# Kernel tuning notes

Hardware: AMD Instinct MI355X
Metric: run time of the kernel (lower is better)

Reference implementation:

```python
import jax, jax.numpy as jnp
import numpy as np

N_NODES = 15
K = 5
L_IN = 1920
C_OUT = 256
L3 = L_IN - 3 * K + 3  # 1908
EPS = 1e-5


def setup_inputs() -> dict:
    key = jax.random.key(0)
    ks = jax.random.split(key, 18)
    B, E = 128, 56
    s = 0.05
    inp = {
        'X': jax.random.normal(ks[0], (B, N_NODES, L_IN), jnp.float32),
        'edge_index': jax.random.randint(ks[1], (2, E), 0, N_NODES),
        'edge_weight': jax.random.uniform(ks[2], (E,), jnp.float32),
        # grouped conv params (groups = N_NODES): per-group channels 1->16->32->1
        'conv1_w': jax.random.normal(ks[3], (16 * N_NODES, 1, K), jnp.float32) * s,
        'conv1_b': jnp.zeros((16 * N_NODES,), jnp.float32),
        'conv2_w': jax.random.normal(ks[4], (32 * N_NODES, 16, K), jnp.float32) * s,
        'conv2_b': jnp.zeros((32 * N_NODES,), jnp.float32),
        'conv3_w': jax.random.normal(ks[5], (N_NODES, 32, K), jnp.float32) * s,
        'conv3_b': jnp.zeros((N_NODES,), jnp.float32),
        # GCNConv: lin weight [out,in] + bias
        'gcn_w': jax.random.normal(ks[6], (C_OUT, L3), jnp.float32) * s,
        'gcn_b': jnp.zeros((C_OUT,), jnp.float32),
        'lin1_w': jax.random.normal(ks[7], (C_OUT, L_IN), jnp.float32) * s,
        'lin1_b': jnp.zeros((C_OUT,), jnp.float32),
        # GraphNorm params
        'gn_w': jnp.ones((C_OUT,), jnp.float32),
        'gn_b': jnp.zeros((C_OUT,), jnp.float32),
        'gn_ms': jnp.ones((C_OUT,), jnp.float32),
        'out_w': jax.random.normal(ks[8], (16, C_OUT), jnp.float32) * s,
        'out_b': jnp.zeros((16,), jnp.float32),
    }
    return inp


def _gconv(x, w, b):
    # grouped valid conv1d, NCH layout
    y = jax.lax.conv_general_dilated(
        x, w, window_strides=(1,), padding='VALID',
        dimension_numbers=('NCH', 'OIH', 'NCH'),
        feature_group_count=N_NODES)
    return y + b[None, :, None]


def _gcn(x, edge_index, edge_weight, W, b):
    # x: [B, N, L3]; batched GCNConv with shared edge structure (no per-t loop)
    src, dst = edge_index[0], edge_index[1]
    loop = jnp.arange(N_NODES)
    src = jnp.concatenate([src, loop])
    dst = jnp.concatenate([dst, loop])
    ew = jnp.concatenate([edge_weight, jnp.ones((N_NODES,), edge_weight.dtype)])
    deg = jnp.zeros((N_NODES,), ew.dtype).at[dst].add(ew)  # in-degree on target
    dinv = jnp.where(deg > 0, jax.lax.rsqrt(deg), 0.0)
    norm = dinv[src] * ew * dinv[dst]  # [E']
    xl = jnp.einsum('bnf,of->bno', x, W)  # [B, N, C_OUT]
    msg = norm[None, :, None] * xl[:, src, :]  # [B, E', C_OUT]
    out = jnp.zeros_like(xl).at[:, dst, :].add(msg)
    return out + b


def reference(X, edge_index, edge_weight, conv1_w, conv1_b, conv2_w, conv2_b,
              conv3_w, conv3_b, gcn_w, gcn_b, lin1_w, lin1_b, gn_w, gn_b,
              gn_ms, out_w, out_b):
    h = jax.nn.leaky_relu(_gconv(X, conv1_w, conv1_b), 0.01)
    h = jax.nn.leaky_relu(_gconv(h, conv2_w, conv2_b), 0.01)
    h = jax.nn.leaky_relu(_gconv(h, conv3_w, conv3_b), 0.01)  # [B, N, L3]
    T = _gcn(h, edge_index, edge_weight, gcn_w, gcn_b)  # [B, N, C_OUT]
    # GraphNorm with batch=None -> single graph over dim 0
    mean = T.mean(axis=0, keepdims=True)
    out = T - mean * gn_ms
    var = (out * out).mean(axis=0, keepdims=True)
    T = gn_w * out / jnp.sqrt(var + EPS) + gn_b
    T = jax.nn.elu(T + jnp.einsum('bnl,ol->bno', X, lin1_w) + lin1_b)
    output = T.mean(axis=1)  # global_mean_pool over nodes -> [B, C_OUT]
    class_output = output @ out_w.T + out_b  # [B, 16]
    return (output, class_output)
```

## Files before the change

kernel.cpp:

```cpp
#include <hip/hip_runtime.h>

typedef unsigned short u16;
typedef unsigned int   u32;

typedef short shortx8   __attribute__((ext_vector_type(8)));
typedef float floatx4   __attribute__((ext_vector_type(4)));
typedef float floatx16  __attribute__((ext_vector_type(16)));
typedef u32   uintx2    __attribute__((ext_vector_type(2)));
typedef u32   uintx4    __attribute__((ext_vector_type(4)));

typedef u32     u32a     __attribute__((may_alias));
typedef uintx2  uintx2a  __attribute__((may_alias));
typedef uintx4  uintx4a  __attribute__((may_alias));
typedef shortx8 shortx8a __attribute__((may_alias));

__device__ __forceinline__ u16 f2bf(float f){
  union { float f; u32 i; } v; v.f = f;
  return (u16)((v.i + 0x7fffu + ((v.i >> 16) & 1u)) >> 16);
}
__device__ __forceinline__ u16 f2bf_fast(float f){
  union { float f; u32 i; } v; v.f = f;
  return (u16)((v.i + 0x8000u) >> 16);
}
__device__ __forceinline__ u32 pack2(float lo, float hi){
  union { float f; u32 i; } a, b; a.f = lo; b.f = hi;
  return __builtin_amdgcn_perm(b.i + 0x8000u, a.i + 0x8000u, 0x07060302u);
}
__device__ __forceinline__ u32 cvtpk2(float lo, float hi){
#if __has_builtin(__builtin_amdgcn_cvt_pk_bf16_f32)
  auto pv = __builtin_amdgcn_cvt_pk_bf16_f32(lo, hi);
  if constexpr (sizeof(pv) == 4){
    u32 out; __builtin_memcpy(&out, &pv, 4); return out;
  } else {
    return pack2(lo, hi);
  }
#else
  return pack2(lo, hi);
#endif
}
__device__ __forceinline__ float lrelu(float v){ return fmaxf(v, 0.01f*v); }

__global__ void __launch_bounds__(256, 4) fused_conv(
    const float* __restrict__ X,
    const float* __restrict__ w1, const float* __restrict__ b1,
    const float* __restrict__ w2, const float* __restrict__ b2,
    const float* __restrict__ w3, const float* __restrict__ b3,
    u16* __restrict__ h3p, u16* __restrict__ Xb,
    const float* __restrict__ lw, u16* __restrict__ lwb,
    const float* __restrict__ gw, u16* __restrict__ gwp,
    float* __restrict__ xlz, float* __restrict__ l1z){
  const int tid  = threadIdx.x;
  const int node = blockIdx.z;
  const int p0   = blockIdx.x * 120;
  const int b0   = blockIdx.y * 8;

  __shared__ __attribute__((aligned(16))) u16 sPair[2][4352];
  __shared__ __attribute__((aligned(16))) u16 sW2f[2560];
  __shared__ __attribute__((aligned(16))) u16 sW3f[160];
  __shared__ __attribute__((aligned(16))) u16 sXb[8*136];
  __shared__ float sW1[80], sB1[16], sB2[32];

  {
    const int bid = blockIdx.x + 16*(blockIdx.y + 16*blockIdx.z);
    int gid = bid*256 + tid;
    if (gid < 491520){
      lwb[gid] = f2bf(lw[gid]);
      xlz[gid] = 0.f;
    } else {
      int g2 = gid - 491520;
      int row = g2 / 1920;
      int col = g2 - row*1920;
      gwp[g2] = (col < 1908) ? f2bf(gw[row*1908 + col]) : (u16)0;
      l1z[g2] = 0.f;
    }
  }

  {
    const int bls = tid >> 5, i0 = tid & 31;
    const float* xrow = X  + (size_t)((b0 + bls)*15 + node)*1920;
    u16*        xbrow = Xb + (size_t)((b0 + bls)*15 + node)*1920;
    #pragma unroll
    for (int u = 0; u < 5; ++u){
      int i = i0 + 32*u;
      if (i < 136){
        int g = p0 + i;
        float xv = (g < 1920) ? xrow[g] : 0.f;
        u16 xb = f2bf_fast(xv);
        sXb[bls*136 + i] = xb;
        if (i < 120) xbrow[g] = xb;
      }
    }
    #pragma unroll
    for (int u = 0; u < 10; ++u){
      int d = tid + 256*u;
      int j = d & 7, oc = (d >> 3) & 31, kh = (d >> 8) & 1, tap = d >> 9;
      sW2f[d] = f2bf(w2[node*2560 + (oc*16 + kh*8 + j)*5 + tap]);
    }
    if (tid < 160){
      int icc = tid / 5, tp = tid - 5*icc;
      sW3f[tp*32 + icc] = f2bf(w3[node*160 + tid]);
    }
    if (tid < 80) sW1[tid] = w1[node*80 + tid];
    if (tid < 16) sB1[tid] = b1[node*16 + tid];
    if (tid < 32) sB2[tid] = b2[node*32 + tid];
    {
      const int pr = tid >> 7, idx = tid & 127;
      sPair[pr][1632 + (64 + (idx >> 5))*40 + (idx & 31)] = 0;
    }
  }
  __syncthreads();

  const int w = tid >> 6, lane = tid & 63;
  const int pw = w >> 1, ph = w & 1;
  const int m = lane & 15, quad = lane >> 4;
  const int t32 = lane & 31, kh = lane >> 5;

  shortx8 a2t[5];
  #pragma unroll
  for (int tap = 0; tap < 5; ++tap)
    a2t[tap] = *(const shortx8a*)&sW2f[((tap*2 + kh)*32 + t32)*8];

  float biasr[16];
  #pragma unroll
  for (int r = 0; r < 16; ++r)
    biasr[r] = sB2[(r&3) + 8*(r>>2) + 4*kh];

  shortx8 a3[5];
  {
    const shortx8 zv = {0,0,0,0,0,0,0,0};
    #pragma unroll
    for (int tp = 0; tp < 5; ++tp){
      shortx8 t = *(const shortx8a*)&sW3f[tp*32 + quad*8];
      a3[tp] = (m == 0) ? t : zv;
    }
  }
  const float b3v = b3[node];

  shortx8 a1h = {0,0,0,0,0,0,0,0}, a1l = {0,0,0,0,0,0,0,0};
  if (quad == 0){
    const float* wrow = sW1 + m*5;
    #pragma unroll
    for (int j = 0; j < 5; ++j){
      float wv = wrow[j];
      u16 h = f2bf(wv);
      union { u32 i; float f; } hf; hf.i = ((u32)h) << 16;
      u16 l = f2bf(wv - hf.f);
      a1h[j] = (short)h; a1l[j] = (short)l;
    }
  }
  float biasA[4];
  #pragma unroll
  for (int r = 0; r < 4; ++r) biasA[r] = sB1[quad*4 + r];

  u16* h1w = sPair[pw];
  u16* h2w = sPair[pw] + 1632;

  for (int bb = 0; bb < 4; ++bb){
    const int bl = pw + bb*2;
    const int rg = (b0 + bl)*15 + node;

    {
      const int s = tid & 127;
      if (s < 68){
        const u32* xb32 = (const u32*)sXb + bl*68;
        u32 r0 = xb32[s];
        u32 r1 = (s+1 < 68) ? xb32[s+1] : 0u;
        u32 r2 = (s+2 < 68) ? xb32[s+2] : 0u;
        u32 r3 = (s+3 < 68) ? xb32[s+3] : 0u;
        u32 r4 = (s+4 < 68) ? xb32[s+4] : 0u;
        const int te = 2*s, to = 2*s + 1;
        const int offE = (s < 34) ? te*24 + 16 : 1632 + (te - 68)*40 + 32;
        const int offO = (s < 34) ? to*24 + 16 : 1632 + (to - 68)*40 + 32;
        uintx4 ve = {r0, r1, r2, r3};
        uintx4 vo = {__builtin_amdgcn_alignbit(r1, r0, 16),
                     __builtin_amdgcn_alignbit(r2, r1, 16),
                     __builtin_amdgcn_alignbit(r3, r2, 16),
                     __builtin_amdgcn_alignbit(r4, r3, 16)};
        *(uintx4a*)(h1w + offE) = ve;
        *(uintx4a*)(h1w + offO) = vo;
      }
    }
    __syncthreads();

    #pragma unroll
    for (int tt = 0; tt < 2; ++tt){
      const int p = p0 + tt*60;

      #pragma unroll
      for (int ti = 0; ti < 3; ++ti){
        const int T = ph + 2*ti;
        if (T < 5){
          const int tr = T*16 + m;
          int row = tt*60 + tr;
          row = row > 135 ? 135 : row;
          shortx8 bfr = {0,0,0,0,0,0,0,0};
          if (quad == 0){
            const int off = (row < 68) ? row*24 + 16 : 1632 + (row - 68)*40 + 32;
            bfr = *(const shortx8a*)(h1w + off);
          }
          floatx4 acc = {biasA[0], biasA[1], biasA[2], biasA[3]};
          acc = __builtin_amdgcn_mfma_f32_16x16x32_bf16(a1l, bfr, acc, 0, 0, 0);
          acc = __builtin_amdgcn_mfma_f32_16x16x32_bf16(a1h, bfr, acc, 0, 0, 0);
          if (tr < 68){
            uintx2 pk = { cvtpk2(lrelu(acc[0]), lrelu(acc[1])),
                          cvtpk2(lrelu(acc[2]), lrelu(acc[3])) };
            *(uintx2a*)(h1w + tr*24 + quad*4) = pk;
          }
        }
      }
      __syncthreads();

      {
        const int t0 = ph*32;
        floatx16 acc;
        #pragma unroll
        for (int r = 0; r < 16; ++r) acc[r] = biasr[r];
        #pragma unroll
        for (int tap = 0; tap < 5; ++tap){
          shortx8 bfr = *(const shortx8a*)(h1w + (t0 + t32 + tap)*24 + kh*8);
          acc = __builtin_amdgcn_mfma_f32_32x32x16_bf16(a2t[tap], bfr, acc, 0, 0, 0);
        }
        u16* dst = h2w + (t0 + t32)*40;
        #pragma unroll
        for (int r = 0; r < 16; r += 2){
          float v0 = lrelu(acc[r]);
          float v1 = lrelu(acc[r+1]);
          const int oc0 = (r&3) + 8*(r>>2) + 4*kh;
          *(u32a*)(dst + oc0) = cvtpk2(v0, v1);
        }
      }
      __syncthreads();

      #pragma unroll
      for (int i = 0; i < 2; ++i){
        const int nt = 2*ph + i;
        floatx4 acc3 = {0.f,0.f,0.f,0.f};
        if (lane < 16) acc3[0] = b3v;
        #pragma unroll
        for (int tp = 0; tp < 5; ++tp){
          shortx8 bfr = *(const shortx8a*)(h2w + (nt*16 + m + tp)*40 + quad*8);
          acc3 = __builtin_amdgcn_mfma_f32_16x16x32_bf16(a3[tp], bfr, acc3, 0, 0, 0);
        }
        const int tl = nt*16 + lane;
        if (lane < 16 && tl < 60){
          const int t3 = p + tl;
          float v = lrelu(acc3[0]);
          h3p[(size_t)rg*1920 + t3] = (t3 < 1908) ? f2bf_fast(v) : (u16)0;
        }
      }
    }
  }
}

__global__ void __launch_bounds__(256) gemm_nt(
    const u16* __restrict__ A0, const u16* __restrict__ B0, float* __restrict__ O0,
    const u16* __restrict__ A1, const u16* __restrict__ B1, float* __restrict__ O1,
    float* __restrict__ gZ){
  const int job = blockIdx.z >> 1, khf = blockIdx.z & 1;
  const u16* A; const u16* Bm; float* O;
  if (job == 0){ A = A0; Bm = B0; O = O0; } else { A = A1; Bm = B1; O = O1; }
  __shared__ __attribute__((aligned(16))) u16 sA[2][64*88];
  __shared__ __attribute__((aligned(16))) u16 sB[2][64*88];
  const int tid = threadIdx.x;
  if (blockIdx.x == 0 && blockIdx.y == 0 && blockIdx.z == 0){
    #pragma unroll
    for (int u = 0; u < 30; ++u) gZ[tid + 256*u] = 0.f;
  }
  const int m0 = blockIdx.x*64, n0 = blockIdx.y*64;
  const int row = tid >> 2, kc = tid & 3;
  const int w = tid >> 6, lane = tid & 63;
  const int m = lane & 15, quad = lane >> 4;
  const int mo = (w & 1)*32, no = (w >> 1)*32;
  floatx4 acc[2][2];
  #pragma unroll
  for (int i = 0; i < 2; ++i)
    #pragma unroll
    for (int j = 0; j < 2; ++j)
      #pragma unroll
      for (int r = 0; r < 4; ++r) acc[i][j][r] = 0.f;

  const u16* ap = A  + (size_t)(m0 + row)*1920 + khf*960 + kc*8;
  const u16* bp = Bm + (size_t)(n0 + row)*1920 + khf*960 + kc*8;
  uintx4 va0 = *(const uintx4a*)ap;
  uintx4 va1 = *(const uintx4a*)(ap + 32);
  uintx4 vb0 = *(const uintx4a*)bp;
  uintx4 vb1 = *(const uintx4a*)(bp + 32);
  ap += 64; bp += 64;

  for (int kt = 0; kt < 15; ++kt){
    const int c = kt & 1;
    *(uintx4a*)&sA[c][row*88 + kc*8]      = va0;
    *(uintx4a*)&sA[c][row*88 + 32 + kc*8] = va1;
    *(uintx4a*)&sB[c][row*88 + kc*8]      = vb0;
    *(uintx4a*)&sB[c][row*88 + 32 + kc*8] = vb1;
    __syncthreads();
    if (kt < 14){
      va0 = *(const uintx4a*)ap;
      va1 = *(const uintx4a*)(ap + 32);
      vb0 = *(const uintx4a*)bp;
      vb1 = *(const uintx4a*)(bp + 32);
      ap += 64; bp += 64;
    }
    #pragma unroll
    for (int ks = 0; ks < 64; ks += 32){
      const shortx8 af0 = *(const shortx8a*)&sA[c][(mo      + m)*88 + ks + quad*8];
      const shortx8 af1 = *(const shortx8a*)&sA[c][(mo + 16 + m)*88 + ks + quad*8];
      const shortx8 bf0 = *(const shortx8a*)&sB[c][(no      + m)*88 + ks + quad*8];
      const shortx8 bf1 = *(const shortx8a*)&sB[c][(no + 16 + m)*88 + ks + quad*8];
      acc[0][0] = __builtin_amdgcn_mfma_f32_16x16x32_bf16(af0, bf0, acc[0][0], 0, 0, 0);
      acc[0][1] = __builtin_amdgcn_mfma_f32_16x16x32_bf16(af0, bf1, acc[0][1], 0, 0, 0);
      acc[1][0] = __builtin_amdgcn_mfma_f32_16x16x32_bf16(af1, bf0, acc[1][0], 0, 0, 0);
      acc[1][1] = __builtin_amdgcn_mfma_f32_16x16x32_bf16(af1, bf1, acc[1][1], 0, 0, 0);
    }
  }
  #pragma unroll
  for (int mi = 0; mi < 2; ++mi)
    #pragma unroll
    for (int ni = 0; ni < 2; ++ni)
      #pragma unroll
      for (int r = 0; r < 4; ++r){
        int rr = m0 + mo + mi*16 + quad*4 + r;
        int cc = n0 + no + ni*16 + m;
        atomicAdd(&O[(size_t)rr*256 + cc], acc[mi][ni][r]);
      }
}

__global__ void __launch_bounds__(256) gcn_agg(
    const float* __restrict__ xl, const int* __restrict__ ei,
    const float* __restrict__ ew, const float* __restrict__ gcn_b,
    float* __restrict__ Tpre, float* __restrict__ gS, float* __restrict__ gS2){
  const int b = blockIdx.x, tid = threadIdx.x;
  __shared__ float sxl[15*256];
  __shared__ float s_deg[15], s_dinv[15], s_norm[71];
  __shared__ int   s_cnt[15], s_start[16], s_fill[15], s_srcl[71];
  if (tid < 15){ s_deg[tid] = 0.f; s_cnt[tid] = 0; s_fill[tid] = 0; }
  #pragma unroll
  for (int n = 0; n < 15; ++n)
    sxl[n*256 + tid] = xl[(size_t)(b*15 + n)*256 + tid];
  __syncthreads();
  int se = 0, de = 0; float we = 0.f;
  if (tid < 71){
    if (tid < 56){ se = ei[tid]; de = ei[56 + tid]; we = ew[tid]; }
    else         { se = tid - 56; de = tid - 56; we = 1.0f; }
    atomicAdd(&s_deg[de], we);
    atomicAdd(&s_cnt[de], 1);
  }
  __syncthreads();
  if (tid < 15) s_dinv[tid] = s_deg[tid] > 0.f ? rsqrtf(s_deg[tid]) : 0.f;
  if (tid == 0){
    int a = 0;
    for (int n = 0; n < 15; ++n){ s_start[n] = a; a += s_cnt[n]; }
    s_start[15] = a;
  }
  __syncthreads();
  if (tid < 71){
    float nrm = s_dinv[se]*we*s_dinv[de];
    int pos = s_start[de] + atomicAdd(&s_fill[de], 1);
    s_srcl[pos] = se; s_norm[pos] = nrm;
  }
  __syncthreads();
  const float gb = gcn_b[tid];
  for (int n = 0; n < 15; ++n){
    float acc = gb;
    const int e0 = s_start[n], e1 = s_start[n+1];
    for (int idx = e0; idx < e1; ++idx)
      acc += s_norm[idx]*sxl[s_srcl[idx]*256 + tid];
    Tpre[(size_t)(b*15 + n)*256 + tid] = acc;
    atomicAdd(&gS [n*256 + tid], acc);
    atomicAdd(&gS2[n*256 + tid], acc*acc);
  }
}

__global__ void __launch_bounds__(256) finalize_k(
    const float* __restrict__ Tpre, const float* __restrict__ l1,
    const float* __restrict__ gS, const float* __restrict__ gS2,
    const float* __restrict__ gn_ms, const float* __restrict__ gn_w,
    const float* __restrict__ gn_b, const float* __restrict__ lin1_b,
    const float* __restrict__ out_w, const float* __restrict__ out_b,
    float* __restrict__ dout){
  const int b = blockIdx.x, tid = threadIdx.x;
  __shared__ float spool[256], spart[256];
  const float gnb = gn_b[tid], lb = lin1_b[tid];
  const float gms = gn_ms[tid], gwc = gn_w[tid];
  float acc = 0.f;
  #pragma unroll
  for (int n = 0; n < 15; ++n){
    const float s  = gS [n*256 + tid];
    const float s2 = gS2[n*256 + tid];
    const float mean = s*(1.f/128.f);
    const float mo   = mean*gms;
    float var = s2*(1.f/128.f) - 2.f*mo*mean + mo*mo;
    var = fmaxf(var, 0.f);
    const float scal = gwc*rsqrtf(var + 1e-5f);
    float t = (Tpre[(size_t)(b*15 + n)*256 + tid] - mo)*scal
              + gnb + l1[(size_t)(b*15 + n)*256 + tid] + lb;
    t = t > 0.f ? t : (__expf(t) - 1.f);
    acc += t;
  }
  const float pool = acc*(1.f/15.f);
  dout[b*256 + tid] = pool;
  spool[tid] = pool;
  __syncthreads();
  const int j = tid >> 4, q = tid & 15;
  float s = 0.f;
  for (int i = 0; i < 16; ++i){
    int cc = q + i*16;
    s += spool[cc]*out_w[j*256 + cc];
  }
  spart[tid] = s;
  __syncthreads();
  if (tid < 16){
    float tot = out_b[tid];
    #pragma unroll
    for (int i = 0; i < 16; ++i) tot += spart[tid*16 + i];
    dout[32768 + b*16 + tid] = tot;
  }
}

extern "C" void kernel_launch(void* const* d_in, const int* in_sizes, int n_in,
                              void* d_out, int out_size, void* d_ws, size_t ws_size,
                              hipStream_t stream){
  (void)in_sizes; (void)n_in; (void)out_size; (void)ws_size;
  const float* X    = (const float*)d_in[0];
  const int*   ei   = (const int*)d_in[1];
  const float* ew   = (const float*)d_in[2];
  const float* w1   = (const float*)d_in[3];
  const float* b1   = (const float*)d_in[4];
  const float* w2   = (const float*)d_in[5];
  const float* b2   = (const float*)d_in[6];
  const float* w3   = (const float*)d_in[7];
  const float* b3   = (const float*)d_in[8];
  const float* gw   = (const float*)d_in[9];
  const float* gb   = (const float*)d_in[10];
  const float* lw   = (const float*)d_in[11];
  const float* lb   = (const float*)d_in[12];
  const float* gnw  = (const float*)d_in[13];
  const float* gnb  = (const float*)d_in[14];
  const float* gnms = (const float*)d_in[15];
  const float* ow   = (const float*)d_in[16];
  const float* ob   = (const float*)d_in[17];

  char* ws = (char*)d_ws;
  u16*   h3p  = (u16*)(ws + 0);
  u16*   gwp  = (u16*)(ws + 7372800);
  u16*   Xb   = (u16*)(ws + 8355840);
  u16*   lwb  = (u16*)(ws + 15728640);
  float* xl   = (float*)(ws + 16711680);
  float* l1   = (float*)(ws + 18677760);
  float* gS   = (float*)(ws + 20643840);
  float* gS2  = (float*)(ws + 20659200);
  float* Tpre = (float*)(ws + 0);

  fused_conv<<<dim3(16, 16, 15), dim3(256), 0, stream>>>(X, w1, b1, w2, b2, w3, b3,
                                                         h3p, Xb, lw, lwb, gw, gwp,
                                                         xl, l1);
  gemm_nt   <<<dim3(30, 4, 4),   dim3(256), 0, stream>>>(Xb, lwb, l1, h3p, gwp, xl, gS);
  gcn_agg   <<<dim3(128),        dim3(256), 0, stream>>>(xl, ei, ew, gb, Tpre, gS, gS2);
  finalize_k<<<dim3(128),        dim3(256), 0, stream>>>(Tpre, l1, gS, gS2,
                                                         gnms, gnw, gnb, lb, ow, ob,
                                                         (float*)d_out);
}
```

Baseline: 193.0 us.

## Fuse GCN aggregation and finalize into one kernel with grid-wide barrier

Merges the GCN aggregation and GraphNorm/ELU/pool/classifier kernels into a single 128-block kernel. The blocks synchronise through a global atomic counter, reset by gemm_nt, before reading the batch statistics. Each block keeps its aggregated rows in shared memory instead of writing and re-reading Tpre, and one kernel launch is removed. The spin barrier assumes all 128 blocks are co-resident, and the fused path is used only when the workspace is large enough, otherwise it falls back to the old two kernels.

```diff
diff --git a/kernel.cpp b/kernel.cpp
--- a/kernel.cpp
+++ b/kernel.cpp
@@ -255,7 +255,7 @@
 __global__ void __launch_bounds__(256) gemm_nt(
     const u16* __restrict__ A0, const u16* __restrict__ B0, float* __restrict__ O0,
     const u16* __restrict__ A1, const u16* __restrict__ B1, float* __restrict__ O1,
-    float* __restrict__ gZ){
+    float* __restrict__ gZ, int* __restrict__ ctr){
   const int job = blockIdx.z >> 1, khf = blockIdx.z & 1;
   const u16* A; const u16* Bm; float* O;
   if (job == 0){ A = A0; Bm = B0; O = O0; } else { A = A1; Bm = B1; O = O1; }
@@ -265,6 +265,7 @@
   if (blockIdx.x == 0 && blockIdx.y == 0 && blockIdx.z == 0){
     #pragma unroll
     for (int u = 0; u < 30; ++u) gZ[tid + 256*u] = 0.f;
+    if (tid == 0 && ctr) *ctr = 0;
   }
   const int m0 = blockIdx.x*64, n0 = blockIdx.y*64;
   const int row = tid >> 2, kc = tid & 3;
@@ -325,6 +326,108 @@
       }
 }
 
+__global__ void __launch_bounds__(256) gcn_finalize(
+    const float* __restrict__ xl, const int* __restrict__ ei,
+    const float* __restrict__ ew, const float* __restrict__ gcn_b,
+    float* __restrict__ gS, float* __restrict__ gS2, int* __restrict__ ctr,
+    const float* __restrict__ l1,
+    const float* __restrict__ gn_ms, const float* __restrict__ gn_w,
+    const float* __restrict__ gn_b, const float* __restrict__ lin1_b,
+    const float* __restrict__ out_w, const float* __restrict__ out_b,
+    float* __restrict__ dout){
+  const int b = blockIdx.x, tid = threadIdx.x;
+  __shared__ float sxl[15*256];
+  __shared__ float sT [15*256];
+  __shared__ float spool[256], spart[256];
+  __shared__ float s_deg[15], s_dinv[15], s_norm[71];
+  __shared__ int   s_cnt[15], s_start[16], s_fill[15], s_srcl[71];
+
+  if (tid < 15){ s_deg[tid] = 0.f; s_cnt[tid] = 0; s_fill[tid] = 0; }
+  #pragma unroll
+  for (int n = 0; n < 15; ++n)
+    sxl[n*256 + tid] = xl[(size_t)(b*15 + n)*256 + tid];
+  __syncthreads();
+  int se = 0, de = 0; float we = 0.f;
+  if (tid < 71){
+    if (tid < 56){ se = ei[tid]; de = ei[56 + tid]; we = ew[tid]; }
+    else         { se = tid - 56; de = tid - 56; we = 1.0f; }
+    atomicAdd(&s_deg[de], we);
+    atomicAdd(&s_cnt[de], 1);
+  }
+  __syncthreads();
+  if (tid < 15) s_dinv[tid] = s_deg[tid] > 0.f ? rsqrtf(s_deg[tid]) : 0.f;
+  if (tid == 0){
+    int a = 0;
+    for (int n = 0; n < 15; ++n){ s_start[n] = a; a += s_cnt[n]; }
+    s_start[15] = a;
+  }
+  __syncthreads();
+  if (tid < 71){
+    float nrm = s_dinv[se]*we*s_dinv[de];
+    int pos = s_start[de] + atomicAdd(&s_fill[de], 1);
+    s_srcl[pos] = se; s_norm[pos] = nrm;
+  }
+  __syncthreads();
+  const float gb = gcn_b[tid];
+  #pragma unroll
+  for (int n = 0; n < 15; ++n){
+    float acc = gb;
+    const int e0 = s_start[n], e1 = s_start[n+1];
+    for (int idx = e0; idx < e1; ++idx)
+      acc += s_norm[idx]*sxl[s_srcl[idx]*256 + tid];
+    sT[n*256 + tid] = acc;
+    atomicAdd(&gS [n*256 + tid], acc);
+    atomicAdd(&gS2[n*256 + tid], acc*acc);
+  }
+
+  __threadfence();
+  __syncthreads();
+  if (tid == 0){
+    __hip_atomic_fetch_add(ctr, 1, __ATOMIC_ACQ_REL, __HIP_MEMORY_SCOPE_AGENT);
+    while (__hip_atomic_load(ctr, __ATOMIC_ACQUIRE, __HIP_MEMORY_SCOPE_AGENT) < 128)
+      __builtin_amdgcn_s_sleep(2);
+  }
+  __syncthreads();
+
+  const float gnb = gn_b[tid], lb = lin1_b[tid];
+  const float gms = gn_ms[tid], gwc = gn_w[tid];
+  float acc = 0.f;
+  #pragma unroll
+  for (int n = 0; n < 15; ++n){
+    const float s  = __hip_atomic_load(&gS [n*256 + tid], __ATOMIC_RELAXED,
+                                       __HIP_MEMORY_SCOPE_AGENT);
+    const float s2 = __hip_atomic_load(&gS2[n*256 + tid], __ATOMIC_RELAXED,
+                                       __HIP_MEMORY_SCOPE_AGENT);
+    const float mean = s*(1.f/128.f);
+    const float mo   = mean*gms;
+    float var = s2*(1.f/128.f) - 2.f*mo*mean + mo*mo;
+    var = fmaxf(var, 0.f);
+    const float scal = gwc*rsqrtf(var + 1e-5f);
+    float t = (sT[n*256 + tid] - mo)*scal
+              + gnb + l1[(size_t)(b*15 + n)*256 + tid] + lb;
+    t = t > 0.f ? t : (__expf(t) - 1.f);
+    acc += t;
+  }
+  const float pool = acc*(1.f/15.f);
+  dout[b*256 + tid] = pool;
+  spool[tid] = pool;
+  __syncthreads();
+  const int j = tid >> 4, q = tid & 15;
+  float s = 0.f;
+  for (int i = 0; i < 16; ++i){
+    int cc = q + i*16;
+    s += spool[cc]*out_w[j*256 + cc];
+  }
+  spart[tid] = s;
+  __syncthreads();
+  if (tid < 16){
+    float tot = out_b[tid];
+    #pragma unroll
+    for (int i = 0; i < 16; ++i) tot += spart[tid*16 + i];
+    dout[32768 + b*16 + tid] = tot;
+  }
+}
+
 __global__ void __launch_bounds__(256) gcn_agg(
     const float* __restrict__ xl, const int* __restrict__ ei,
     const float* __restrict__ ew, const float* __restrict__ gcn_b,
@@ -420,7 +523,7 @@
 extern "C" void kernel_launch(void* const* d_in, const int* in_sizes, int n_in,
                               void* d_out, int out_size, void* d_ws, size_t ws_size,
                               hipStream_t stream){
-  (void)in_sizes; (void)n_in; (void)out_size; (void)ws_size;
+  (void)in_sizes; (void)n_in; (void)out_size;
   const float* X    = (const float*)d_in[0];
   const int*   ei   = (const int*)d_in[1];
   const float* ew   = (const float*)d_in[2];
@@ -450,13 +553,22 @@
   float* gS   = (float*)(ws + 20643840);
   float* gS2  = (float*)(ws + 20659200);
   float* Tpre = (float*)(ws + 0);
+  const bool fused_tail = ws_size >= 20674560 + 64;
+  int*   ctr  = fused_tail ? (int*)(ws + 20674560) : (int*)nullptr;
 
   fused_conv<<<dim3(16, 16, 15), dim3(256), 0, stream>>>(X, w1, b1, w2, b2, w3, b3,
                                                          h3p, Xb, lw, lwb, gw, gwp,
                                                          xl, l1);
-  gemm_nt   <<<dim3(30, 4, 4),   dim3(256), 0, stream>>>(Xb, lwb, l1, h3p, gwp, xl, gS);
-  gcn_agg   <<<dim3(128),        dim3(256), 0, stream>>>(xl, ei, ew, gb, Tpre, gS, gS2);
-  finalize_k<<<dim3(128),        dim3(256), 0, stream>>>(Tpre, l1, gS, gS2,
-                                                         gnms, gnw, gnb, lb, ow, ob,
-                                                         (float*)d_out);
-}
+  gemm_nt   <<<dim3(30, 4, 4),   dim3(256), 0, stream>>>(Xb, lwb, l1, h3p, gwp, xl,
+                                                         gS, ctr);
+  if (fused_tail){
+    gcn_finalize<<<dim3(128), dim3(256), 0, stream>>>(xl, ei, ew, gb, gS, gS2, ctr,
+                                                      l1, gnms, gnw, gnb, lb, ow, ob,
+                                                      (float*)d_out);
+  } else {
+    gcn_agg   <<<dim3(128), dim3(256), 0, stream>>>(xl, ei, ew, gb, Tpre, gS, gS2);
+    finalize_k<<<dim3(128), dim3(256), 0, stream>>>(Tpre, l1, gS, gS2,
+                                                    gnms, gnw, gnb, lb, ow, ob,
+                                                    (float*)d_out);
+  }
+}
```

New measurement: 205.2 us. +6.3%, slower.
